# Performance work log

Hardware: AMD Instinct MI355X
Metric: run time of the kernel (lower is better)

## Reference

```python
import jax, jax.numpy as jnp
import numpy as np

B, T, C, H = 8, 2048, 1024, 128  # batch, seq (=block_size), n_embd, head_size


def setup_inputs() -> dict:
    key = jax.random.key(0)
    kx, kk, kq, kv = jax.random.split(key, 4)
    x = jax.random.normal(kx, (B, T, C), dtype=jnp.float32)
    # nn.Linear(n_embd, head_size, bias=False) weights, stored as (in, out) for x @ W
    s = 1.0 / np.sqrt(C)
    Wk = jax.random.normal(kk, (C, H), dtype=jnp.float32) * s
    Wq = jax.random.normal(kq, (C, H), dtype=jnp.float32) * s
    Wv = jax.random.normal(kv, (C, H), dtype=jnp.float32) * s
    return {"x": x, "Wk": Wk, "Wq": Wq, "Wv": Wv}


def reference(x, Wk, Wq, Wv):
    # x: [B, T, C]
    Bx, Tx, Cx = x.shape
    k = x @ Wk  # [B, T, H]
    q = x @ Wq  # [B, T, H]
    v = x @ Wv  # [B, T, H]
    # NOTE: source multiplies by C**0.5 (not 1/sqrt), kept faithfully
    wei = jnp.einsum("bth,bsh->bts", q, k) * (Cx ** 0.5)  # [B, T, T]
    causal = jnp.tril(jnp.ones((Tx, Tx), dtype=bool))
    wei = jnp.where(causal, wei, -jnp.inf)
    wei = jax.nn.softmax(wei, axis=-1)
    # dropout omitted (eval-mode reference)
    return wei @ v  # [B, T, H]
```

## Files before the change

### kernel.cpp

```cpp
#include <hip/hip_runtime.h>

constexpr int kB = 8;
constexpr int kT = 2048;
constexpr int kC = 1024;
constexpr int kH = 128;
constexpr int kM = kB * kT;
constexpr size_t kMH = (size_t)kM * kH;
constexpr size_t kWH = (size_t)kC * kH;

#define QSCALE 46.166241308446828f

typedef __attribute__((ext_vector_type(8))) short bf16x8;
typedef __attribute__((ext_vector_type(4))) float f32x4;


__device__ inline unsigned short f2bf_rne(float f) {
    union { float f; unsigned int u; } x; x.f = f;
    unsigned int r = x.u + 0x7fff + ((x.u >> 16) & 1);
    return (unsigned short)(r >> 16);
}
__device__ inline float bf2f(unsigned short h) {
    union { float f; unsigned int u; } x; x.u = ((unsigned int)h) << 16;
    return x.f;
}
__device__ inline unsigned int pack_hi2(float a, float b) {
    return __builtin_amdgcn_perm(__float_as_uint(b), __float_as_uint(a),
                                 0x07060302u);
}
__device__ inline float hi_part(float v) {
    return __uint_as_float(__float_as_uint(v) & 0xffff0000u);
}
__device__ inline void load_lds16(const unsigned short* g, unsigned short* l) {
    __builtin_amdgcn_global_load_lds(
        (const __attribute__((address_space(1))) unsigned int*)g,
        (__attribute__((address_space(3))) unsigned int*)l, 16, 0, 0);
}

__global__ __launch_bounds__(256) void prep_w(
    const float* __restrict__ Wk, const float* __restrict__ Wq,
    const float* __restrict__ Wv, unsigned short* __restrict__ ws)
{
    const int h = blockIdx.x;
    const int mat = blockIdx.y;
    const float* W = (mat == 0) ? Wq : (mat == 1) ? Wk : Wv;
    unsigned short* hi = ws + 5 * kMH + (size_t)(mat * 2) * kWH;
    unsigned short* lo = hi + kWH;

    const int k0 = threadIdx.x * 4;
    unsigned short hv[4], lv[4];
#pragma unroll
    for (int j = 0; j < 4; ++j) {
        const float f = W[(size_t)(k0 + j) * kH + h];
        hv[j] = f2bf_rne(f);
        lv[j] = f2bf_rne(f - bf2f(hv[j]));
    }
    *(uint2*)&hi[(size_t)h * kC + k0] =
        make_uint2(((unsigned)hv[1] << 16) | hv[0], ((unsigned)hv[3] << 16) | hv[2]);
    *(uint2*)&lo[(size_t)h * kC + k0] =
        make_uint2(((unsigned)lv[1] << 16) | lv[0], ((unsigned)lv[3] << 16) | lv[2]);
}

__global__ __launch_bounds__(256) void qkv_mfma(
    const float* __restrict__ x, unsigned short* __restrict__ ws)
{
    __shared__ __align__(16) unsigned short Bh[128 * 64];
    __shared__ __align__(16) unsigned short Bl[128 * 64];

    const int idx = blockIdx.x;
    const int mat = idx >> 8;
    const int m0 = (idx & 255) * 64;
    const unsigned short* wThi = ws + 5 * kMH + (size_t)(mat * 2) * kWH;
    const unsigned short* wTlo = wThi + kWH;

    const int tid = threadIdx.x;
    const int w = tid >> 6, lane = tid & 63;
    const int li = lane & 15, quad = lane >> 4;

    const float* xrow = x + (size_t)(m0 + w * 16 + li) * kC;

    f32x4 acc[8];
#pragma unroll
    for (int j = 0; j < 8; ++j) acc[j] = (f32x4){0.f, 0.f, 0.f, 0.f};

    for (int kt = 0; kt < kC; kt += 64) {
        if (kt) __syncthreads();
#pragma unroll
        for (int u = 0; u < 4; ++u) {
            const int f = u * 256 + tid;
            const int row = f >> 3, g = (f & 7) ^ (row & 7);
            load_lds16(wThi + (size_t)row * kC + kt + g * 8, Bh + f * 8);
            if (mat <= 1)
                load_lds16(wTlo + (size_t)row * kC + kt + g * 8, Bl + f * 8);
        }
        float4 xa[2][2];
#pragma unroll
        for (int kc = 0; kc < 2; ++kc) {
            xa[kc][0] = *(const float4*)(xrow + kt + kc * 32 + quad * 8);
            xa[kc][1] = *(const float4*)(xrow + kt + kc * 32 + quad * 8 + 4);
        }
        bf16x8 ah[2], al[2];
        if (mat <= 1) {
#pragma unroll
            for (int kc = 0; kc < 2; ++kc) {
                const float4 a0 = xa[kc][0], a1 = xa[kc][1];
                unsigned int hp[4], lp[4];
                hp[0] = pack_hi2(a0.x, a0.y); hp[1] = pack_hi2(a0.z, a0.w);
                hp[2] = pack_hi2(a1.x, a1.y); hp[3] = pack_hi2(a1.z, a1.w);
                lp[0] = pack_hi2(a0.x - hi_part(a0.x), a0.y - hi_part(a0.y));
                lp[1] = pack_hi2(a0.z - hi_part(a0.z), a0.w - hi_part(a0.w));
                lp[2] = pack_hi2(a1.x - hi_part(a1.x), a1.y - hi_part(a1.y));
                lp[3] = pack_hi2(a1.z - hi_part(a1.z), a1.w - hi_part(a1.w));
                ah[kc] = *(bf16x8*)hp;
                al[kc] = *(bf16x8*)lp;
            }
        } else {
#pragma unroll
            for (int kc = 0; kc < 2; ++kc) {
                const float4 a0 = xa[kc][0], a1 = xa[kc][1];
                unsigned short e[8];
                e[0] = f2bf_rne(a0.x); e[1] = f2bf_rne(a0.y);
                e[2] = f2bf_rne(a0.z); e[3] = f2bf_rne(a0.w);
                e[4] = f2bf_rne(a1.x); e[5] = f2bf_rne(a1.y);
                e[6] = f2bf_rne(a1.z); e[7] = f2bf_rne(a1.w);
                ah[kc] = *(bf16x8*)e;
            }
        }
        __syncthreads();

        if (mat <= 1) {
#pragma unroll
            for (int kc = 0; kc < 2; ++kc)
#pragma unroll
                for (int nt = 0; nt < 8; ++nt) {
                    const int row = nt * 16 + li;
                    const int pos = (kc * 4 + quad) ^ (row & 7);
                    const bf16x8 bh = *(const bf16x8*)&Bh[row * 64 + pos * 8];
                    const bf16x8 bl = *(const bf16x8*)&Bl[row * 64 + pos * 8];
                    acc[nt] = __builtin_amdgcn_mfma_f32_16x16x32_bf16(ah[kc], bh, acc[nt], 0, 0, 0);
                    acc[nt] = __builtin_amdgcn_mfma_f32_16x16x32_bf16(al[kc], bh, acc[nt], 0, 0, 0);
                    acc[nt] = __builtin_amdgcn_mfma_f32_16x16x32_bf16(ah[kc], bl, acc[nt], 0, 0, 0);
                }
        } else {
#pragma unroll
            for (int kc = 0; kc < 2; ++kc)
#pragma unroll
                for (int nt = 0; nt < 8; ++nt) {
                    const int row = nt * 16 + li;
                    const int pos = (kc * 4 + quad) ^ (row & 7);
                    const bf16x8 bh = *(const bf16x8*)&Bh[row * 64 + pos * 8];
                    acc[nt] = __builtin_amdgcn_mfma_f32_16x16x32_bf16(ah[kc], bh, acc[nt], 0, 0, 0);
                }
        }
    }

    if (mat <= 1) {
        unsigned short* hip_ = ws + (size_t)(mat * 2) * kMH;
        unsigned short* lop  = hip_ + kMH;
        const float sc = (mat == 0) ? QSCALE : 1.0f;
#pragma unroll
        for (int nt = 0; nt < 8; ++nt) {
            const int col = nt * 16 + li;
#pragma unroll
            for (int reg = 0; reg < 4; ++reg) {
                const int row = m0 + w * 16 + quad * 4 + reg;
                const float v = acc[nt][reg] * sc;
                hip_[(size_t)row * kH + col] = (unsigned short)(__float_as_uint(v) >> 16);
                lop[(size_t)row * kH + col] =
                    (unsigned short)(__float_as_uint(v - hi_part(v)) >> 16);
            }
        }
    } else {
        unsigned short* vt = ws + 4 * kMH;
        const int bb = m0 >> 11;
        const int t0 = (m0 & (kT - 1)) + w * 16 + quad * 4;
#pragma unroll
        for (int nt = 0; nt < 8; ++nt) {
            const int h = nt * 16 + li;
            ushort4 pk;
            pk.x = f2bf_rne(acc[nt][0]);
            pk.y = f2bf_rne(acc[nt][1]);
            pk.z = f2bf_rne(acc[nt][2]);
            pk.w = f2bf_rne(acc[nt][3]);
            *(ushort4*)&vt[((size_t)(bb * kH + h)) * kT + t0] = pk;
        }
    }
}

__global__ __launch_bounds__(256, 2) void attn_mfma(
    const unsigned short* __restrict__ ws, float* __restrict__ out)
{
    __shared__ __align__(16) unsigned short Ps[4][2][16][40];
    __shared__ __align__(16) float Ml[4][32][2];
    __shared__ __align__(16) float Obuf[3][32][128];

    const int tid = threadIdx.x;
    const int w = tid >> 6, lane = tid & 63;
    const int li = lane & 15, quad = lane >> 4;

    const int idx = blockIdx.x;
    const int b = idx & 7;
    const int j = idx >> 3;
    const int qt = (j < 32) ? j : 95 - j;
    const int i0 = qt * 32;
    const int nc = qt + 1;

    const unsigned short* qhi = ws;
    const unsigned short* qlo = ws + kMH;
    const unsigned short* khi = ws + 2 * kMH;
    const unsigned short* klo = ws + 3 * kMH;
    const unsigned short* vt  = ws + 4 * kMH;

    bf16x8 qh[2][4], ql[2][4];
#pragma unroll
    for (int mi = 0; mi < 2; ++mi) {
        const size_t qoff = ((size_t)(b * kT + i0 + mi * 16 + li)) * kH;
#pragma unroll
        for (int kc = 0; kc < 4; ++kc) {
            qh[mi][kc] = *(const bf16x8*)(qhi + qoff + kc * 32 + quad * 8);
            ql[mi][kc] = *(const bf16x8*)(qlo + qoff + kc * 32 + quad * 8);
        }
    }

    f32x4 o[2][8];
#pragma unroll
    for (int mi = 0; mi < 2; ++mi)
#pragma unroll
        for (int ht = 0; ht < 8; ++ht) o[mi][ht] = (f32x4){0.f, 0.f, 0.f, 0.f};
    float m_i[2][4], l_i[2][4];
#pragma unroll
    for (int mi = 0; mi < 2; ++mi)
#pragma unroll
        for (int reg = 0; reg < 4; ++reg) { m_i[mi][reg] = -3.0e38f; l_i[mi][reg] = 0.f; }

    for (int jc = w; jc < nc; jc += 4) {
        const int t0 = jc * 32;
        bf16x8 vf[8];
#pragma unroll
        for (int ht = 0; ht < 8; ++ht)
            vf[ht] = *(const bf16x8*)(vt + (size_t)(b * kH + ht * 16 + li) * kT +
                                      t0 + quad * 8);
        f32x4 s[2][2];
#pragma unroll
        for (int mi = 0; mi < 2; ++mi)
#pragma unroll
            for (int nt = 0; nt < 2; ++nt) s[mi][nt] = (f32x4){0.f, 0.f, 0.f, 0.f};
#pragma unroll
        for (int kc = 0; kc < 4; ++kc) {
            bf16x8 kh[2], kl[2];
#pragma unroll
            for (int nt = 0; nt < 2; ++nt) {
                const size_t ka =
                    ((size_t)(b * kT + t0 + nt * 16 + li)) * kH + kc * 32 + quad * 8;
                kh[nt] = *(const bf16x8*)(khi + ka);
                kl[nt] = *(const bf16x8*)(klo + ka);
            }
#pragma unroll
            for (int mi = 0; mi < 2; ++mi)
#pragma unroll
                for (int nt = 0; nt < 2; ++nt) {
                    s[mi][nt] = __builtin_amdgcn_mfma_f32_16x16x32_bf16(qh[mi][kc], kh[nt], s[mi][nt], 0, 0, 0);
                    s[mi][nt] = __builtin_amdgcn_mfma_f32_16x16x32_bf16(ql[mi][kc], kh[nt], s[mi][nt], 0, 0, 0);
                    s[mi][nt] = __builtin_amdgcn_mfma_f32_16x16x32_bf16(qh[mi][kc], kl[nt], s[mi][nt], 0, 0, 0);
                }
        }
        if (jc == qt) {
#pragma unroll
            for (int mi = 0; mi < 2; ++mi) {
                const int grow0 = i0 + mi * 16 + quad * 4;
#pragma unroll
                for (int nt = 0; nt < 2; ++nt) {
                    const int gcol = t0 + nt * 16 + li;
#pragma unroll
                    for (int reg = 0; reg < 4; ++reg)
                        if (gcol > grow0 + reg) s[mi][nt][reg] = -3.0e38f;
                }
            }
        }
#pragma unroll
        for (int mi = 0; mi < 2; ++mi) {
            float alpha[4];
#pragma unroll
            for (int reg = 0; reg < 4; ++reg) {
                float mr = fmaxf(s[mi][0][reg], s[mi][1][reg]);
                mr = fmaxf(mr, __shfl_xor(mr, 1));
                mr = fmaxf(mr, __shfl_xor(mr, 2));
                mr = fmaxf(mr, __shfl_xor(mr, 4));
                mr = fmaxf(mr, __shfl_xor(mr, 8));
                const float mn = fmaxf(m_i[mi][reg], mr);
                alpha[reg] = exp2f(m_i[mi][reg] - mn);
                m_i[mi][reg] = mn;
                const float p0 = exp2f(s[mi][0][reg] - mn);
                const float p1 = exp2f(s[mi][1][reg] - mn);
                s[mi][0][reg] = p0; s[mi][1][reg] = p1;
                float rs = p0 + p1;
                rs += __shfl_xor(rs, 1);
                rs += __shfl_xor(rs, 2);
                rs += __shfl_xor(rs, 4);
                rs += __shfl_xor(rs, 8);
                l_i[mi][reg] = l_i[mi][reg] * alpha[reg] + rs;
            }
            const f32x4 av = {alpha[0], alpha[1], alpha[2], alpha[3]};
#pragma unroll
            for (int ht = 0; ht < 8; ++ht) o[mi][ht] *= av;
#pragma unroll
            for (int nt = 0; nt < 2; ++nt)
#pragma unroll
                for (int reg = 0; reg < 4; ++reg)
                    Ps[w][mi][quad * 4 + reg][nt * 16 + li] = f2bf_rne(s[mi][nt][reg]);
        }
#pragma unroll
        for (int mi = 0; mi < 2; ++mi) {
            const bf16x8 pf = *(const bf16x8*)&Ps[w][mi][li][quad * 8];
#pragma unroll
            for (int ht = 0; ht < 8; ++ht)
                o[mi][ht] = __builtin_amdgcn_mfma_f32_16x16x32_bf16(pf, vf[ht], o[mi][ht], 0, 0, 0);
        }
    }

    if (li == 0) {
#pragma unroll
        for (int mi = 0; mi < 2; ++mi)
#pragma unroll
            for (int reg = 0; reg < 4; ++reg) {
                Ml[w][mi * 16 + quad * 4 + reg][0] = m_i[mi][reg];
                Ml[w][mi * 16 + quad * 4 + reg][1] = l_i[mi][reg];
            }
    }
    __syncthreads();
    float a_self[2][4], linv[2][4];
#pragma unroll
    for (int mi = 0; mi < 2; ++mi)
#pragma unroll
        for (int reg = 0; reg < 4; ++reg) {
            const int row = mi * 16 + quad * 4 + reg;
            const float m0_ = Ml[0][row][0], m1 = Ml[1][row][0];
            const float m2 = Ml[2][row][0], m3 = Ml[3][row][0];
            const float ms = fmaxf(fmaxf(m0_, m1), fmaxf(m2, m3));
            const float L = Ml[0][row][1] * exp2f(m0_ - ms) +
                            Ml[1][row][1] * exp2f(m1 - ms) +
                            Ml[2][row][1] * exp2f(m2 - ms) +
                            Ml[3][row][1] * exp2f(m3 - ms);
            a_self[mi][reg] = exp2f(m_i[mi][reg] - ms);
            linv[mi][reg] = 1.0f / L;
        }
    if (w) {
#pragma unroll
        for (int mi = 0; mi < 2; ++mi)
#pragma unroll
            for (int ht = 0; ht < 8; ++ht)
#pragma unroll
                for (int reg = 0; reg < 4; ++reg)
                    Obuf[w - 1][mi * 16 + quad * 4 + reg][ht * 16 + li] =
                        o[mi][ht][reg] * a_self[mi][reg];
    }
    __syncthreads();
    if (w == 0) {
#pragma unroll
        for (int mi = 0; mi < 2; ++mi)
#pragma unroll
            for (int ht = 0; ht < 8; ++ht)
#pragma unroll
                for (int reg = 0; reg < 4; ++reg) {
                    const int row = mi * 16 + quad * 4 + reg;
                    const int col = ht * 16 + li;
                    const float v = o[mi][ht][reg] * a_self[mi][reg] +
                                    Obuf[0][row][col] + Obuf[1][row][col] +
                                    Obuf[2][row][col];
                    out[(size_t)(b * kT + i0 + row) * kH + col] = v * linv[mi][reg];
                }
    }
}

extern "C" void kernel_launch(void* const* d_in, const int* in_sizes, int n_in,
                              void* d_out, int out_size, void* d_ws, size_t ws_size,
                              hipStream_t stream) {
    const float* x  = (const float*)d_in[0];
    const float* Wk = (const float*)d_in[1];
    const float* Wq = (const float*)d_in[2];
    const float* Wv = (const float*)d_in[3];
    unsigned short* ws = (unsigned short*)d_ws;
    float* out = (float*)d_out;

    hipLaunchKernelGGL(prep_w, dim3(128, 3), dim3(256), 0, stream, Wk, Wq, Wv, ws);
    hipLaunchKernelGGL(qkv_mfma, dim3(768), dim3(256), 0, stream, x, ws);
    hipLaunchKernelGGL(attn_mfma, dim3(512), dim3(256), 0, stream,
                       (const unsigned short*)ws, out);
}
```

Measured before the change: 196.7 us.

## Halve attention query tile to 16 rows, double grid, prefetch K fragments

The attention kernel now gives each block 16 query rows instead of 32, which doubles the grid to 1024 blocks and raises launch bounds to 3 blocks per CU. Per-thread state (Q fragments, O accumulators, softmax stats) and shared memory are halved to allow the higher occupancy. K fragments are double-buffered across the head-dim chunks so the next loads are issued before the current MFMAs. The trade-off is that each K/V chunk is now loaded by twice as many blocks, so there is less reuse and more global/L2 traffic per unit of work.

```diff
diff --git a/kernel.cpp b/kernel.cpp
--- a/kernel.cpp
+++ b/kernel.cpp
@@ -186,12 +186,12 @@
     }
 }
 
-__global__ __launch_bounds__(256, 2) void attn_mfma(
+__global__ __launch_bounds__(256, 3) void attn_mfma(
     const unsigned short* __restrict__ ws, float* __restrict__ out)
 {
-    __shared__ __align__(16) unsigned short Ps[4][2][16][40];
-    __shared__ __align__(16) float Ml[4][32][2];
-    __shared__ __align__(16) float Obuf[3][32][128];
+    __shared__ __align__(16) unsigned short Ps[4][16][40];
+    __shared__ __align__(16) float Ml[4][16][2];
+    __shared__ __align__(16) float Obuf[3][16][128];
 
     const int tid = threadIdx.x;
     const int w = tid >> 6, lane = tid & 63;
@@ -200,9 +200,10 @@
     const int idx = blockIdx.x;
     const int b = idx & 7;
     const int j = idx >> 3;
-    const int qt = (j < 32) ? j : 95 - j;
-    const int i0 = qt * 32;
-    const int nc = qt + 1;
+    const int qt = (j < 64) ? j : 191 - j;
+    const int i0 = qt * 16;
+    const int nc = (qt >> 1) + 1;
+    const int jd = qt >> 1;
 
     const unsigned short* qhi = ws;
     const unsigned short* qlo = ws + kMH;
@@ -210,27 +211,22 @@
     const unsigned short* klo = ws + 3 * kMH;
     const unsigned short* vt  = ws + 4 * kMH;
 
-    bf16x8 qh[2][4], ql[2][4];
-#pragma unroll
-    for (int mi = 0; mi < 2; ++mi) {
-        const size_t qoff = ((size_t)(b * kT + i0 + mi * 16 + li)) * kH;
+    bf16x8 qh[4], ql[4];
+    {
+        const size_t qoff = ((size_t)(b * kT + i0 + li)) * kH;
 #pragma unroll
         for (int kc = 0; kc < 4; ++kc) {
-            qh[mi][kc] = *(const bf16x8*)(qhi + qoff + kc * 32 + quad * 8);
-            ql[mi][kc] = *(const bf16x8*)(qlo + qoff + kc * 32 + quad * 8);
-        }
-    }
-
-    f32x4 o[2][8];
-#pragma unroll
-    for (int mi = 0; mi < 2; ++mi)
-#pragma unroll
-        for (int ht = 0; ht < 8; ++ht) o[mi][ht] = (f32x4){0.f, 0.f, 0.f, 0.f};
-    float m_i[2][4], l_i[2][4];
-#pragma unroll
-    for (int mi = 0; mi < 2; ++mi)
-#pragma unroll
-        for (int reg = 0; reg < 4; ++reg) { m_i[mi][reg] = -3.0e38f; l_i[mi][reg] = 0.f; }
+            qh[kc] = *(const bf16x8*)(qhi + qoff + kc * 32 + quad * 8);
+            ql[kc] = *(const bf16x8*)(qlo + qoff + kc * 32 + quad * 8);
+        }
+    }
+
+    f32x4 o[8];
+#pragma unroll
+    for (int ht = 0; ht < 8; ++ht) o[ht] = (f32x4){0.f, 0.f, 0.f, 0.f};
+    float m_i[4], l_i[4];
+#pragma unroll
+    for (int reg = 0; reg < 4; ++reg) { m_i[reg] = -3.0e38f; l_i[reg] = 0.f; }
 
     for (int jc = w; jc < nc; jc += 4) {
         const int t0 = jc * 32;
@@ -239,135 +235,124 @@
         for (int ht = 0; ht < 8; ++ht)
             vf[ht] = *(const bf16x8*)(vt + (size_t)(b * kH + ht * 16 + li) * kT +
                                       t0 + quad * 8);
-        f32x4 s[2][2];
-#pragma unroll
-        for (int mi = 0; mi < 2; ++mi)
-#pragma unroll
-            for (int nt = 0; nt < 2; ++nt) s[mi][nt] = (f32x4){0.f, 0.f, 0.f, 0.f};
+        f32x4 s[2];
+        s[0] = (f32x4){0.f, 0.f, 0.f, 0.f};
+        s[1] = (f32x4){0.f, 0.f, 0.f, 0.f};
+        bf16x8 kh[2][2], kl[2][2];
+#pragma unroll
+        for (int nt = 0; nt < 2; ++nt) {
+            const size_t ka =
+                ((size_t)(b * kT + t0 + nt * 16 + li)) * kH + quad * 8;
+            kh[0][nt] = *(const bf16x8*)(khi + ka);
+            kl[0][nt] = *(const bf16x8*)(klo + ka);
+        }
 #pragma unroll
         for (int kc = 0; kc < 4; ++kc) {
-            bf16x8 kh[2], kl[2];
+            const int cur = kc & 1, nxt = cur ^ 1;
+            if (kc < 3) {
+#pragma unroll
+                for (int nt = 0; nt < 2; ++nt) {
+                    const size_t ka = ((size_t)(b * kT + t0 + nt * 16 + li)) * kH +
+                                      (kc + 1) * 32 + quad * 8;
+                    kh[nxt][nt] = *(const bf16x8*)(khi + ka);
+                    kl[nxt][nt] = *(const bf16x8*)(klo + ka);
+                }
+            }
 #pragma unroll
             for (int nt = 0; nt < 2; ++nt) {
-                const size_t ka =
-                    ((size_t)(b * kT + t0 + nt * 16 + li)) * kH + kc * 32 + quad * 8;
-                kh[nt] = *(const bf16x8*)(khi + ka);
-                kl[nt] = *(const bf16x8*)(klo + ka);
-            }
-#pragma unroll
-            for (int mi = 0; mi < 2; ++mi)
-#pragma unroll
-                for (int nt = 0; nt < 2; ++nt) {
-                    s[mi][nt] = __builtin_amdgcn_mfma_f32_16x16x32_bf16(qh[mi][kc], kh[nt], s[mi][nt], 0, 0, 0);
-                    s[mi][nt] = __builtin_amdgcn_mfma_f32_16x16x32_bf16(ql[mi][kc], kh[nt], s[mi][nt], 0, 0, 0);
-                    s[mi][nt] = __builtin_amdgcn_mfma_f32_16x16x32_bf16(qh[mi][kc], kl[nt], s[mi][nt], 0, 0, 0);
-                }
-        }
-        if (jc == qt) {
-#pragma unroll
-            for (int mi = 0; mi < 2; ++mi) {
-                const int grow0 = i0 + mi * 16 + quad * 4;
-#pragma unroll
-                for (int nt = 0; nt < 2; ++nt) {
-                    const int gcol = t0 + nt * 16 + li;
-#pragma unroll
-                    for (int reg = 0; reg < 4; ++reg)
-                        if (gcol > grow0 + reg) s[mi][nt][reg] = -3.0e38f;
-                }
-            }
-        }
-#pragma unroll
-        for (int mi = 0; mi < 2; ++mi) {
-            float alpha[4];
-#pragma unroll
-            for (int reg = 0; reg < 4; ++reg) {
-                float mr = fmaxf(s[mi][0][reg], s[mi][1][reg]);
-                mr = fmaxf(mr, __shfl_xor(mr, 1));
-                mr = fmaxf(mr, __shfl_xor(mr, 2));
-                mr = fmaxf(mr, __shfl_xor(mr, 4));
-                mr = fmaxf(mr, __shfl_xor(mr, 8));
-                const float mn = fmaxf(m_i[mi][reg], mr);
-                alpha[reg] = exp2f(m_i[mi][reg] - mn);
-                m_i[mi][reg] = mn;
-                const float p0 = exp2f(s[mi][0][reg] - mn);
-                const float p1 = exp2f(s[mi][1][reg] - mn);
-                s[mi][0][reg] = p0; s[mi][1][reg] = p1;
-                float rs = p0 + p1;
-                rs += __shfl_xor(rs, 1);
-                rs += __shfl_xor(rs, 2);
-                rs += __shfl_xor(rs, 4);
-                rs += __shfl_xor(rs, 8);
-                l_i[mi][reg] = l_i[mi][reg] * alpha[reg] + rs;
-            }
-            const f32x4 av = {alpha[0], alpha[1], alpha[2], alpha[3]};
-#pragma unroll
-            for (int ht = 0; ht < 8; ++ht) o[mi][ht] *= av;
-#pragma unroll
-            for (int nt = 0; nt < 2; ++nt)
+                s[nt] = __builtin_amdgcn_mfma_f32_16x16x32_bf16(qh[kc], kh[cur][nt], s[nt], 0, 0, 0);
+                s[nt] = __builtin_amdgcn_mfma_f32_16x16x32_bf16(ql[kc], kh[cur][nt], s[nt], 0, 0, 0);
+                s[nt] = __builtin_amdgcn_mfma_f32_16x16x32_bf16(qh[kc], kl[cur][nt], s[nt], 0, 0, 0);
+            }
+        }
+        if (jc == jd) {
+            const int grow0 = i0 + quad * 4;
+#pragma unroll
+            for (int nt = 0; nt < 2; ++nt) {
+                const int gcol = t0 + nt * 16 + li;
 #pragma unroll
                 for (int reg = 0; reg < 4; ++reg)
-                    Ps[w][mi][quad * 4 + reg][nt * 16 + li] = f2bf_rne(s[mi][nt][reg]);
-        }
-#pragma unroll
-        for (int mi = 0; mi < 2; ++mi) {
-            const bf16x8 pf = *(const bf16x8*)&Ps[w][mi][li][quad * 8];
-#pragma unroll
-            for (int ht = 0; ht < 8; ++ht)
-                o[mi][ht] = __builtin_amdgcn_mfma_f32_16x16x32_bf16(pf, vf[ht], o[mi][ht], 0, 0, 0);
-        }
+                    if (gcol > grow0 + reg) s[nt][reg] = -3.0e38f;
+            }
+        }
+        float alpha[4];
+#pragma unroll
+        for (int reg = 0; reg < 4; ++reg) {
+            float mr = fmaxf(s[0][reg], s[1][reg]);
+            mr = fmaxf(mr, __shfl_xor(mr, 1));
+            mr = fmaxf(mr, __shfl_xor(mr, 2));
+            mr = fmaxf(mr, __shfl_xor(mr, 4));
+            mr = fmaxf(mr, __shfl_xor(mr, 8));
+            const float mn = fmaxf(m_i[reg], mr);
+            alpha[reg] = exp2f(m_i[reg] - mn);
+            m_i[reg] = mn;
+            const float p0 = exp2f(s[0][reg] - mn);
+            const float p1 = exp2f(s[1][reg] - mn);
+            s[0][reg] = p0; s[1][reg] = p1;
+            float rs = p0 + p1;
+            rs += __shfl_xor(rs, 1);
+            rs += __shfl_xor(rs, 2);
+            rs += __shfl_xor(rs, 4);
+            rs += __shfl_xor(rs, 8);
+            l_i[reg] = l_i[reg] * alpha[reg] + rs;
+        }
+        const f32x4 av = {alpha[0], alpha[1], alpha[2], alpha[3]};
+#pragma unroll
+        for (int ht = 0; ht < 8; ++ht) o[ht] *= av;
+#pragma unroll
+        for (int nt = 0; nt < 2; ++nt)
+#pragma unroll
+            for (int reg = 0; reg < 4; ++reg)
+                Ps[w][quad * 4 + reg][nt * 16 + li] = f2bf_rne(s[nt][reg]);
+        const bf16x8 pf = *(const bf16x8*)&Ps[w][li][quad * 8];
+#pragma unroll
+        for (int ht = 0; ht < 8; ++ht)
+            o[ht] = __builtin_amdgcn_mfma_f32_16x16x32_bf16(pf, vf[ht], o[ht], 0, 0, 0);
     }
 
     if (li == 0) {
 #pragma unroll
-        for (int mi = 0; mi < 2; ++mi)
-#pragma unroll
-            for (int reg = 0; reg < 4; ++reg) {
-                Ml[w][mi * 16 + quad * 4 + reg][0] = m_i[mi][reg];
-                Ml[w][mi * 16 + quad * 4 + reg][1] = l_i[mi][reg];
-            }
+        for (int reg = 0; reg < 4; ++reg) {
+            Ml[w][quad * 4 + reg][0] = m_i[reg];
+            Ml[w][quad * 4 + reg][1] = l_i[reg];
+        }
     }
     __syncthreads();
-    float a_self[2][4], linv[2][4];
-#pragma unroll
-    for (int mi = 0; mi < 2; ++mi)
-#pragma unroll
-        for (int reg = 0; reg < 4; ++reg) {
-            const int row = mi * 16 + quad * 4 + reg;
-            const float m0_ = Ml[0][row][0], m1 = Ml[1][row][0];
-            const float m2 = Ml[2][row][0], m3 = Ml[3][row][0];
-            const float ms = fmaxf(fmaxf(m0_, m1), fmaxf(m2, m3));
-            const float L = Ml[0][row][1] * exp2f(m0_ - ms) +
-                            Ml[1][row][1] * exp2f(m1 - ms) +
-                            Ml[2][row][1] * exp2f(m2 - ms) +
-                            Ml[3][row][1] * exp2f(m3 - ms);
-            a_self[mi][reg] = exp2f(m_i[mi][reg] - ms);
-            linv[mi][reg] = 1.0f / L;
-        }
+    float a_self[4], linv[4];
+#pragma unroll
+    for (int reg = 0; reg < 4; ++reg) {
+        const int row = quad * 4 + reg;
+        const float m0_ = Ml[0][row][0], m1 = Ml[1][row][0];
+        const float m2 = Ml[2][row][0], m3 = Ml[3][row][0];
+        const float ms = fmaxf(fmaxf(m0_, m1), fmaxf(m2, m3));
+        const float L = Ml[0][row][1] * exp2f(m0_ - ms) +
+                        Ml[1][row][1] * exp2f(m1 - ms) +
+                        Ml[2][row][1] * exp2f(m2 - ms) +
+                        Ml[3][row][1] * exp2f(m3 - ms);
+        a_self[reg] = exp2f(m_i[reg] - ms);
+        linv[reg] = 1.0f / L;
+    }
     if (w) {
 #pragma unroll
-        for (int mi = 0; mi < 2; ++mi)
-#pragma unroll
-            for (int ht = 0; ht < 8; ++ht)
-#pragma unroll
-                for (int reg = 0; reg < 4; ++reg)
-                    Obuf[w - 1][mi * 16 + quad * 4 + reg][ht * 16 + li] =
-                        o[mi][ht][reg] * a_self[mi][reg];
+        for (int ht = 0; ht < 8; ++ht)
+#pragma unroll
+            for (int reg = 0; reg < 4; ++reg)
+                Obuf[w - 1][quad * 4 + reg][ht * 16 + li] =
+                    o[ht][reg] * a_self[reg];
     }
     __syncthreads();
     if (w == 0) {
 #pragma unroll
-        for (int mi = 0; mi < 2; ++mi)
-#pragma unroll
-            for (int ht = 0; ht < 8; ++ht)
-#pragma unroll
-                for (int reg = 0; reg < 4; ++reg) {
-                    const int row = mi * 16 + quad * 4 + reg;
-                    const int col = ht * 16 + li;
-                    const float v = o[mi][ht][reg] * a_self[mi][reg] +
-                                    Obuf[0][row][col] + Obuf[1][row][col] +
-                                    Obuf[2][row][col];
-                    out[(size_t)(b * kT + i0 + row) * kH + col] = v * linv[mi][reg];
-                }
+        for (int ht = 0; ht < 8; ++ht)
+#pragma unroll
+            for (int reg = 0; reg < 4; ++reg) {
+                const int row = quad * 4 + reg;
+                const int col = ht * 16 + li;
+                const float v = o[ht][reg] * a_self[reg] +
+                                Obuf[0][row][col] + Obuf[1][row][col] +
+                                Obuf[2][row][col];
+                out[(size_t)(b * kT + i0 + row) * kH + col] = v * linv[reg];
+            }
     }
 }
 
@@ -383,6 +368,6 @@
 
     hipLaunchKernelGGL(prep_w, dim3(128, 3), dim3(256), 0, stream, Wk, Wq, Wv, ws);
     hipLaunchKernelGGL(qkv_mfma, dim3(768), dim3(256), 0, stream, x, ws);
-    hipLaunchKernelGGL(attn_mfma, dim3(512), dim3(256), 0, stream,
+    hipLaunchKernelGGL(attn_mfma, dim3(1024), dim3(256), 0, stream,
                        (const unsigned short*)ws, out);
 }
```

Measured after the change: 228.9 us. +16.4%, slower.
